# Kernel tuning notes

Hardware: AMD Instinct MI355X
Metric: run time of the kernel (lower is better)

Reference implementation:

```python
import jax, jax.numpy as jnp
import numpy as np

N_NODES = 50000
N_EDGES = 800000
F_IN = 128
HIDDEN = 128
N_CLASSES = 40


def setup_inputs() -> dict:
    key = jax.random.key(0)
    ks = jax.random.split(key, 8)
    x = jax.random.normal(ks[0], (N_NODES, F_IN), dtype=jnp.float32)
    edge_index = jax.random.randint(ks[1], (2, N_EDGES), 0, N_NODES, dtype=jnp.int32)
    s_in = 1.0 / np.sqrt(F_IN)
    s_h = 1.0 / np.sqrt(HIDDEN)
    W1_l = jax.random.normal(ks[2], (F_IN, HIDDEN), jnp.float32) * s_in
    W1_r = jax.random.normal(ks[3], (F_IN, HIDDEN), jnp.float32) * s_in
    b1 = jnp.zeros((HIDDEN,), jnp.float32)
    W2_l = jax.random.normal(ks[4], (HIDDEN, N_CLASSES), jnp.float32) * s_h
    W2_r = jax.random.normal(ks[5], (HIDDEN, N_CLASSES), jnp.float32) * s_h
    b2 = jnp.zeros((N_CLASSES,), jnp.float32)
    return {"x": x, "edge_index": edge_index, "W1_l": W1_l, "W1_r": W1_r,
            "b1": b1, "W2_l": W2_l, "W2_r": W2_r, "b2": b2}


def _sage_conv(x, src, dst, W_l, W_r, b):
    # mean-aggregate neighbor features at dst, then linear transform + root weight
    msg = x[src]                                                  # [E, d] gather
    agg = jax.ops.segment_sum(msg, dst, num_segments=N_NODES)     # [N, d] scatter-add
    deg = jax.ops.segment_sum(jnp.ones((src.shape[0],), x.dtype), dst,
                              num_segments=N_NODES)
    agg = agg / jnp.maximum(deg, 1.0)[:, None]                    # mean aggregation
    return agg @ W_l + x @ W_r + b


def reference(x, edge_index, W1_l, W1_r, b1, W2_l, W2_r, b2):
    src, dst = edge_index[0], edge_index[1]
    h = jax.nn.relu(_sage_conv(x, src, dst, W1_l, W1_r, b1))
    # F.dropout(p=0.5, training=self.training) -> identity in eval mode
    out = jax.nn.relu(_sage_conv(h, src, dst, W2_l, W2_r, b2))
    return jax.nn.log_softmax(out, axis=-1)
```

## Files before the change

kernel.cpp:

```cpp
#include <hip/hip_runtime.h>

#define N_NODES 50000
#define N_EDGES 800000
#define F_IN 128
#define HIDDEN 128
#define N_CLASSES 40

#define NBUCKET 391
#define BUCKET_CAP 4096
#define BINA_CHUNK 2048
#define BINA_NBLK 391
#define PREP_ITEMS (N_NODES * 32 + 128 * 256 + 80 * 128)
#define PREP_NBLK (PREP_ITEMS / 256)

#define OFF_RS     0
#define OFF_BCNT   50004
#define OFF_INVDEG 100004
#define OFF_SRCS   150004
#define OFF_AB     950004
#define OFF_PB     950004
#define OFF_Q      2950004
#define OFF_BINS   7350004
#define OFF_WT1    10550004
#define OFF_WT2    10566388

typedef short bf16x8 __attribute__((ext_vector_type(8)));
typedef float f32x4 __attribute__((ext_vector_type(4)));
typedef unsigned short u16x8 __attribute__((ext_vector_type(8)));

static __device__ __forceinline__ unsigned short f2bf(float f) {
  unsigned int u = __builtin_bit_cast(unsigned int, f);
  u = (u + 0x7fffu + ((u >> 16) & 1u)) >> 16;
  return (unsigned short)u;
}
static __device__ __forceinline__ float bf2f(unsigned short s) {
  unsigned int u = ((unsigned int)s) << 16;
  return __builtin_bit_cast(float, u);
}

__global__ __launch_bounds__(256) void k_binA_prep(
    const int* __restrict__ src, const int* __restrict__ dst,
    int* __restrict__ bcnt, int* __restrict__ bins,
    const float* __restrict__ x, const float* __restrict__ W1l,
    const float* __restrict__ W1r, const float* __restrict__ W2l,
    const float* __restrict__ W2r, unsigned short* __restrict__ Ab,
    unsigned short* __restrict__ Wt1, unsigned short* __restrict__ Wt2) {
  if (blockIdx.x >= BINA_NBLK) {
    int idx = (blockIdx.x - BINA_NBLK) * 256 + threadIdx.x;
    if (idx < N_NODES * 32) {
      int row = idx >> 5, c4 = (idx & 31) << 2;
      const float4 v = *(const float4*)(x + (size_t)row * F_IN + c4);
      ushort4 o;
      o.x = f2bf(v.x); o.y = f2bf(v.y); o.z = f2bf(v.z); o.w = f2bf(v.w);
      *(ushort4*)(Ab + (size_t)row * 256 + 128 + c4) = o;
      return;
    }
    idx -= N_NODES * 32;
    if (idx < 128 * 256) {
      int n = idx >> 8, k = idx & 255;
      float v = (k < 128) ? W1l[(size_t)k * 128 + n]
                          : W1r[(size_t)(k - 128) * 128 + n];
      Wt1[(size_t)n * 256 + k] = f2bf(v);
    } else if (idx < 128 * 256 + 80 * 128) {
      int j = idx - 128 * 256;
      int n = j >> 7, k = j & 127;
      float v = (n < 40) ? W2l[(size_t)k * 40 + n]
                         : W2r[(size_t)k * 40 + (n - 40)];
      Wt2[(size_t)n * 128 + k] = f2bf(v);
    }
    return;
  }
  __shared__ int cnt[NBUCKET];
  __shared__ int excl[NBUCKET];
  __shared__ int cursor[NBUCKET];
  __shared__ int bbase[NBUCKET];
  __shared__ int sc[256];
  __shared__ int stage[BINA_CHUNK];
  __shared__ unsigned short bkt[BINA_CHUNK];
  int t = threadIdx.x;
  int e0 = blockIdx.x * BINA_CHUNK;
  int ne = N_EDGES - e0;
  if (ne > BINA_CHUNK) ne = BINA_CHUNK;
  for (int i = t; i < NBUCKET; i += 256) cnt[i] = 0;
  __syncthreads();
  for (int i = t; i < ne; i += 256) atomicAdd(&cnt[dst[e0 + i] >> 7], 1);
  __syncthreads();
  int a = (2 * t < NBUCKET) ? cnt[2 * t] : 0;
  int b2_ = (2 * t + 1 < NBUCKET) ? cnt[2 * t + 1] : 0;
  int s = a + b2_;
  sc[t] = s;
  __syncthreads();
  for (int off = 1; off < 256; off <<= 1) {
    int add = (t >= off) ? sc[t - off] : 0;
    __syncthreads();
    sc[t] += add;
    __syncthreads();
  }
  int pbase = sc[t] - s;
  if (2 * t < NBUCKET) { excl[2 * t] = pbase; cursor[2 * t] = pbase; }
  if (2 * t + 1 < NBUCKET) {
    excl[2 * t + 1] = pbase + a;
    cursor[2 * t + 1] = pbase + a;
  }
  for (int i = t; i < NBUCKET; i += 256)
    bbase[i] = atomicAdd(&bcnt[i], cnt[i]);
  __syncthreads();
  for (int i = t; i < ne; i += 256) {
    int d = dst[e0 + i];
    int sv = src[e0 + i];
    int b = d >> 7;
    int pos = atomicAdd(&cursor[b], 1);
    stage[pos] = ((d & 127) << 16) | sv;
    bkt[pos] = (unsigned short)b;
  }
  __syncthreads();
  for (int i = t; i < ne; i += 256) {
    int b = bkt[i];
    bins[(size_t)b * BUCKET_CAP + bbase[b] + (i - excl[b])] = stage[i];
  }
}

__global__ __launch_bounds__(256) void k_binB(
    const int* __restrict__ bcnt, const int* __restrict__ bins,
    int* __restrict__ rs, int* __restrict__ srcs,
    float* __restrict__ invdeg) {
  __shared__ int sc[256];
  __shared__ int hist[128];
  __shared__ int cursor[128];
  int b = blockIdx.x;
  int t = threadIdx.x;
  int v = 0;
  if (t < b) v += bcnt[t];
  if (t + 256 < b) v += bcnt[t + 256];
  sc[t] = v;
  __syncthreads();
  for (int off = 128; off; off >>= 1) {
    if (t < off) sc[t] += sc[t + off];
    __syncthreads();
  }
  int base = sc[0];
  int cnt = bcnt[b];
  const int* bb = bins + (size_t)b * BUCKET_CAP;
  if (t < 128) hist[t] = 0;
  __syncthreads();
  for (int i = t; i < cnt; i += 256) atomicAdd(&hist[bb[i] >> 16], 1);
  __syncthreads();
  int c = (t < 128) ? hist[t] : 0;
  sc[t] = c;
  __syncthreads();
  for (int off = 1; off < 128; off <<= 1) {
    int add = (t >= off) ? sc[t - off] : 0;
    __syncthreads();
    sc[t] += add;
    __syncthreads();
  }
  int lexcl = sc[t] - c;
  int node = b * 128 + t;
  if (t < 128 && node < N_NODES) {
    rs[node] = base + lexcl;
    invdeg[node] = 1.0f / (float)(c > 1 ? c : 1);
  }
  if (b == 0 && t == 0) rs[N_NODES] = N_EDGES;
  if (t < 128) cursor[t] = lexcl;
  __syncthreads();
  for (int i = t; i < cnt; i += 256) {
    int v2 = bb[i];
    int pos = atomicAdd(&cursor[v2 >> 16], 1);
    srcs[base + pos] = v2 & 0xFFFF;
  }
}

__global__ __launch_bounds__(256) void k_gather1(
    const int* __restrict__ rs, const int* __restrict__ srcs,
    const float* __restrict__ invdeg, unsigned short* __restrict__ Ab) {
  int node = blockIdx.x * 4 + (threadIdx.x >> 6);
  int lane = threadIdx.x & 63;
  int slot = lane >> 3, li = lane & 7;
  if (node >= N_NODES) return;
  int beg = rs[node], end = rs[node + 1];
  float acc[16];
#pragma unroll
  for (int j = 0; j < 16; j++) acc[j] = 0.f;
  for (int i = beg + slot; i < end; i += 8) {
    int s = srcs[i];
    const unsigned short* rp = Ab + (size_t)s * 256 + 128 + li * 8;
    u16x8 v0 = *(const u16x8*)rp;
    u16x8 v1 = *(const u16x8*)(rp + 64);
#pragma unroll
    for (int j = 0; j < 8; j++) {
      acc[j] += bf2f(v0[j]);
      acc[8 + j] += bf2f(v1[j]);
    }
  }
#pragma unroll
  for (int off = 8; off <= 32; off <<= 1)
#pragma unroll
    for (int j = 0; j < 16; j++) acc[j] += __shfl_xor(acc[j], off, 64);
  if (slot == 0) {
    float inv = invdeg[node];
    u16x8 o0, o1;
#pragma unroll
    for (int j = 0; j < 8; j++) {
      o0[j] = f2bf(acc[j] * inv);
      o1[j] = f2bf(acc[8 + j] * inv);
    }
    *(u16x8*)(Ab + (size_t)node * 256 + li * 8) = o0;
    *(u16x8*)(Ab + (size_t)node * 256 + 64 + li * 8) = o1;
  }
}

__global__ __launch_bounds__(256) void k_mlp(
    const unsigned short* __restrict__ Ab, const unsigned short* __restrict__ Wt1,
    const unsigned short* __restrict__ Wt2, const float* __restrict__ b1,
    const float* __restrict__ b2, unsigned short* __restrict__ pb,
    float* __restrict__ q) {
  __shared__ unsigned short hs[64 * 132];
  int w = threadIdx.x >> 6, lane = threadIdx.x & 63;
  int r = lane & 15, quad = lane >> 4;
  int row0 = blockIdx.x * 64 + w * 16;
  int arow = row0 + r;
  if (arow >= N_NODES) arow = N_NODES - 1;
  const unsigned short* Ap = Ab + (size_t)arow * 256 + quad * 8;
  const unsigned short* Bp = Wt1 + (size_t)r * 256 + quad * 8;
  f32x4 acc[8];
#pragma unroll
  for (int n = 0; n < 8; n++) acc[n] = (f32x4){0.f, 0.f, 0.f, 0.f};
#pragma unroll
  for (int k0 = 0; k0 < 256; k0 += 32) {
    bf16x8 af = *(const bf16x8*)(Ap + k0);
#pragma unroll
    for (int n = 0; n < 8; n++) {
      bf16x8 bv = *(const bf16x8*)(Bp + (size_t)n * 16 * 256 + k0);
      acc[n] = __builtin_amdgcn_mfma_f32_16x16x32_bf16(af, bv, acc[n], 0, 0, 0);
    }
  }
  int lrow0 = w * 16 + quad * 4;
#pragma unroll
  for (int n = 0; n < 8; n++) {
    int col = n * 16 + r;
    float bias = b1[col];
#pragma unroll
    for (int reg = 0; reg < 4; reg++)
      hs[(lrow0 + reg) * 132 + col] = f2bf(fmaxf(acc[n][reg] + bias, 0.f));
  }
  __syncthreads();
  int lr = w * 16 + r;
  const unsigned short* Bp2 = Wt2 + (size_t)r * 128 + quad * 8;
  f32x4 acc2[5];
#pragma unroll
  for (int n = 0; n < 5; n++) acc2[n] = (f32x4){0.f, 0.f, 0.f, 0.f};
#pragma unroll
  for (int k0 = 0; k0 < 128; k0 += 32) {
    const unsigned short* hp = &hs[lr * 132 + k0 + quad * 8];
    ushort4 h0 = *(const ushort4*)hp;
    ushort4 h1 = *(const ushort4*)(hp + 4);
    bf16x8 af;
    af[0] = (short)h0.x; af[1] = (short)h0.y; af[2] = (short)h0.z; af[3] = (short)h0.w;
    af[4] = (short)h1.x; af[5] = (short)h1.y; af[6] = (short)h1.z; af[7] = (short)h1.w;
#pragma unroll
    for (int n = 0; n < 5; n++) {
      bf16x8 bv = *(const bf16x8*)(Bp2 + (size_t)n * 16 * 128 + k0);
      acc2[n] = __builtin_amdgcn_mfma_f32_16x16x32_bf16(af, bv, acc2[n], 0, 0, 0);
    }
  }
  int crow0 = row0 + quad * 4;
#pragma unroll
  for (int n = 0; n < 5; n++) {
    int col = n * 16 + r;
#pragma unroll
    for (int reg = 0; reg < 4; reg++) {
      int row = crow0 + reg;
      if (row < N_NODES) {
        float v = acc2[n][reg];
        if (col < N_CLASSES)
          pb[(size_t)row * 40 + col] = f2bf(v);
        else
          q[(size_t)row * N_CLASSES + (col - N_CLASSES)] = v + b2[col - N_CLASSES];
      }
    }
  }
}

__global__ __launch_bounds__(256) void k_final(
    const unsigned short* __restrict__ pb, const float* __restrict__ q,
    const int* __restrict__ rs, const int* __restrict__ srcs,
    const float* __restrict__ invdeg, float* __restrict__ out) {
  int node = blockIdx.x * 4 + (threadIdx.x >> 6);
  int lane = threadIdx.x & 63;
  int slot = lane >> 3, li = lane & 7;
  if (node >= N_NODES) return;
  bool valid = li < 5;
  int beg = rs[node], end = rs[node + 1];
  float acc[8];
#pragma unroll
  for (int j = 0; j < 8; j++) acc[j] = 0.f;
  for (int i = beg + slot; i < end; i += 8) {
    int s = srcs[i];
    if (valid) {
      u16x8 v = *(const u16x8*)(pb + (size_t)s * 40 + li * 8);
#pragma unroll
      for (int j = 0; j < 8; j++) acc[j] += bf2f(v[j]);
    }
  }
#pragma unroll
  for (int off = 8; off <= 32; off <<= 1)
#pragma unroll
    for (int j = 0; j < 8; j++) acc[j] += __shfl_xor(acc[j], off, 64);
  float inv = invdeg[node];
  float v[8];
  float m = -1e30f;
  if (valid) {
    const float* qr = q + (size_t)node * N_CLASSES + li * 8;
    float4 q0 = *(const float4*)qr;
    float4 q1 = *(const float4*)(qr + 4);
    v[0] = fmaxf(acc[0] * inv + q0.x, 0.f);
    v[1] = fmaxf(acc[1] * inv + q0.y, 0.f);
    v[2] = fmaxf(acc[2] * inv + q0.z, 0.f);
    v[3] = fmaxf(acc[3] * inv + q0.w, 0.f);
    v[4] = fmaxf(acc[4] * inv + q1.x, 0.f);
    v[5] = fmaxf(acc[5] * inv + q1.y, 0.f);
    v[6] = fmaxf(acc[6] * inv + q1.z, 0.f);
    v[7] = fmaxf(acc[7] * inv + q1.w, 0.f);
#pragma unroll
    for (int j = 0; j < 8; j++) m = fmaxf(m, v[j]);
  }
#pragma unroll
  for (int off = 1; off <= 4; off <<= 1) m = fmaxf(m, __shfl_xor(m, off, 8));
  float ssum = 0.f;
  if (valid) {
#pragma unroll
    for (int j = 0; j < 8; j++) ssum += __expf(v[j] - m);
  }
#pragma unroll
  for (int off = 1; off <= 4; off <<= 1) ssum += __shfl_xor(ssum, off, 8);
  float lse = __logf(ssum) + m;
  if (slot == 0 && valid) {
    float* orow = out + (size_t)node * N_CLASSES + li * 8;
    *(float4*)orow = make_float4(v[0] - lse, v[1] - lse, v[2] - lse, v[3] - lse);
    *(float4*)(orow + 4) =
        make_float4(v[4] - lse, v[5] - lse, v[6] - lse, v[7] - lse);
  }
}

extern "C" void kernel_launch(void* const* d_in, const int* in_sizes, int n_in,
                              void* d_out, int out_size, void* d_ws,
                              size_t ws_size, hipStream_t stream) {
  const float* x   = (const float*)d_in[0];
  const int*   ei  = (const int*)d_in[1];
  const int*   src = ei;
  const int*   dst = ei + N_EDGES;
  const float* W1l = (const float*)d_in[2];
  const float* W1r = (const float*)d_in[3];
  const float* b1  = (const float*)d_in[4];
  const float* W2l = (const float*)d_in[5];
  const float* W2r = (const float*)d_in[6];
  const float* b2  = (const float*)d_in[7];
  float* out = (float*)d_out;

  float* wsf = (float*)d_ws;
  int*   rs     = (int*)wsf + OFF_RS;
  int*   bcnt   = (int*)wsf + OFF_BCNT;
  float* invdeg = wsf + OFF_INVDEG;
  int*   srcs   = (int*)wsf + OFF_SRCS;
  unsigned short* Ab  = (unsigned short*)(wsf + OFF_AB);
  unsigned short* pb  = (unsigned short*)(wsf + OFF_PB);
  unsigned short* Wt1 = (unsigned short*)(wsf + OFF_WT1);
  unsigned short* Wt2 = (unsigned short*)(wsf + OFF_WT2);
  int*   bins   = (int*)wsf + OFF_BINS;
  float* q = wsf + OFF_Q;

  hipMemsetAsync(bcnt, 0, NBUCKET * sizeof(int), stream);

  k_binA_prep<<<BINA_NBLK + PREP_NBLK, 256, 0, stream>>>(
      src, dst, bcnt, bins, x, W1l, W1r, W2l, W2r, Ab, Wt1, Wt2);
  k_binB<<<NBUCKET, 256, 0, stream>>>(bcnt, bins, rs, srcs, invdeg);
  k_gather1<<<(N_NODES + 3) / 4, 256, 0, stream>>>(rs, srcs, invdeg, Ab);
  k_mlp<<<(N_NODES + 63) / 64, 256, 0, stream>>>(Ab, Wt1, Wt2, b1, b2, pb, q);
  k_final<<<(N_NODES + 3) / 4, 256, 0, stream>>>(pb, q, rs, srcs, invdeg, out);
}
```

Measured before the change: 233.4 us.

## Retile MLP kernel across waves by column and move pb/q off Ab

The fused MLP kernel now handles 32 rows per block, with each wave computing two 16-column tiles for both 16-row tiles. This cuts per-wave weight fragment loads and doubles the block count. The second-layer GEMM is split across waves by row tile and column group. The pb and q outputs move from a region aliasing the Ab input into the spent bins region, which removes a cross-block read/write overlap.

After: 223.2 us. 1.05x faster.

```diff
diff --git a/kernel.cpp b/kernel.cpp
--- a/kernel.cpp
+++ b/kernel.cpp
@@ -18,9 +18,9 @@
 #define OFF_INVDEG 100004
 #define OFF_SRCS   150004
 #define OFF_AB     950004
-#define OFF_PB     950004
-#define OFF_Q      2950004
 #define OFF_BINS   7350004
+#define OFF_PB     7350004
+#define OFF_Q      8350004
 #define OFF_WT1    10550004
 #define OFF_WT2    10566388
 
@@ -214,68 +214,83 @@
     const unsigned short* __restrict__ Wt2, const float* __restrict__ b1,
     const float* __restrict__ b2, unsigned short* __restrict__ pb,
     float* __restrict__ q) {
-  __shared__ unsigned short hs[64 * 132];
+  __shared__ unsigned short hs[32 * 132];
   int w = threadIdx.x >> 6, lane = threadIdx.x & 63;
   int r = lane & 15, quad = lane >> 4;
-  int row0 = blockIdx.x * 64 + w * 16;
-  int arow = row0 + r;
-  if (arow >= N_NODES) arow = N_NODES - 1;
-  const unsigned short* Ap = Ab + (size_t)arow * 256 + quad * 8;
-  const unsigned short* Bp = Wt1 + (size_t)r * 256 + quad * 8;
-  f32x4 acc[8];
-#pragma unroll
-  for (int n = 0; n < 8; n++) acc[n] = (f32x4){0.f, 0.f, 0.f, 0.f};
+  int row0 = blockIdx.x * 32;
+  int ar0 = row0 + r;
+  int ar1 = row0 + 16 + r;
+  if (ar0 >= N_NODES) ar0 = N_NODES - 1;
+  if (ar1 >= N_NODES) ar1 = N_NODES - 1;
+  const unsigned short* Ap0 = Ab + (size_t)ar0 * 256 + quad * 8;
+  const unsigned short* Ap1 = Ab + (size_t)ar1 * 256 + quad * 8;
+  const unsigned short* Bp = Wt1 + (size_t)(w * 32 + r) * 256 + quad * 8;
+  f32x4 acc[2][2];
+#pragma unroll
+  for (int nn = 0; nn < 2; nn++)
+#pragma unroll
+    for (int rt = 0; rt < 2; rt++) acc[nn][rt] = (f32x4){0.f, 0.f, 0.f, 0.f};
 #pragma unroll
   for (int k0 = 0; k0 < 256; k0 += 32) {
-    bf16x8 af = *(const bf16x8*)(Ap + k0);
-#pragma unroll
-    for (int n = 0; n < 8; n++) {
-      bf16x8 bv = *(const bf16x8*)(Bp + (size_t)n * 16 * 256 + k0);
-      acc[n] = __builtin_amdgcn_mfma_f32_16x16x32_bf16(af, bv, acc[n], 0, 0, 0);
-    }
-  }
-  int lrow0 = w * 16 + quad * 4;
-#pragma unroll
-  for (int n = 0; n < 8; n++) {
-    int col = n * 16 + r;
+    bf16x8 a0 = *(const bf16x8*)(Ap0 + k0);
+    bf16x8 a1 = *(const bf16x8*)(Ap1 + k0);
+#pragma unroll
+    for (int nn = 0; nn < 2; nn++) {
+      bf16x8 bv = *(const bf16x8*)(Bp + (size_t)nn * 16 * 256 + k0);
+      acc[nn][0] = __builtin_amdgcn_mfma_f32_16x16x32_bf16(a0, bv, acc[nn][0], 0, 0, 0);
+      acc[nn][1] = __builtin_amdgcn_mfma_f32_16x16x32_bf16(a1, bv, acc[nn][1], 0, 0, 0);
+    }
+  }
+#pragma unroll
+  for (int nn = 0; nn < 2; nn++) {
+    int col = (w * 2 + nn) * 16 + r;
     float bias = b1[col];
 #pragma unroll
-    for (int reg = 0; reg < 4; reg++)
-      hs[(lrow0 + reg) * 132 + col] = f2bf(fmaxf(acc[n][reg] + bias, 0.f));
-  }
-  __syncthreads();
-  int lr = w * 16 + r;
-  const unsigned short* Bp2 = Wt2 + (size_t)r * 128 + quad * 8;
-  f32x4 acc2[5];
-#pragma unroll
-  for (int n = 0; n < 5; n++) acc2[n] = (f32x4){0.f, 0.f, 0.f, 0.f};
+    for (int rt = 0; rt < 2; rt++)
+#pragma unroll
+      for (int reg = 0; reg < 4; reg++)
+        hs[(rt * 16 + quad * 4 + reg) * 132 + col] =
+            f2bf(fmaxf(acc[nn][rt][reg] + bias, 0.f));
+  }
+  __syncthreads();
+  int rt2 = w & 1, ng = w >> 1;
+  int nbeg = ng ? 3 : 0;
+  int ncnt = ng ? 2 : 3;
+  const unsigned short* hrow = hs + (rt2 * 16 + r) * 132 + quad * 8;
+  const unsigned short* Bp2 = Wt2 + (size_t)(nbeg * 16 + r) * 128 + quad * 8;
+  f32x4 acc2[3];
+#pragma unroll
+  for (int j = 0; j < 3; j++) acc2[j] = (f32x4){0.f, 0.f, 0.f, 0.f};
 #pragma unroll
   for (int k0 = 0; k0 < 128; k0 += 32) {
-    const unsigned short* hp = &hs[lr * 132 + k0 + quad * 8];
-    ushort4 h0 = *(const ushort4*)hp;
-    ushort4 h1 = *(const ushort4*)(hp + 4);
+    ushort4 h0 = *(const ushort4*)(hrow + k0);
+    ushort4 h1 = *(const ushort4*)(hrow + k0 + 4);
     bf16x8 af;
     af[0] = (short)h0.x; af[1] = (short)h0.y; af[2] = (short)h0.z; af[3] = (short)h0.w;
     af[4] = (short)h1.x; af[5] = (short)h1.y; af[6] = (short)h1.z; af[7] = (short)h1.w;
 #pragma unroll
-    for (int n = 0; n < 5; n++) {
-      bf16x8 bv = *(const bf16x8*)(Bp2 + (size_t)n * 16 * 128 + k0);
-      acc2[n] = __builtin_amdgcn_mfma_f32_16x16x32_bf16(af, bv, acc2[n], 0, 0, 0);
-    }
-  }
-  int crow0 = row0 + quad * 4;
-#pragma unroll
-  for (int n = 0; n < 5; n++) {
-    int col = n * 16 + r;
-#pragma unroll
-    for (int reg = 0; reg < 4; reg++) {
-      int row = crow0 + reg;
-      if (row < N_NODES) {
-        float v = acc2[n][reg];
-        if (col < N_CLASSES)
-          pb[(size_t)row * 40 + col] = f2bf(v);
-        else
-          q[(size_t)row * N_CLASSES + (col - N_CLASSES)] = v + b2[col - N_CLASSES];
+    for (int j = 0; j < 3; j++) {
+      if (j < ncnt) {
+        bf16x8 bv = *(const bf16x8*)(Bp2 + (size_t)j * 16 * 128 + k0);
+        acc2[j] = __builtin_amdgcn_mfma_f32_16x16x32_bf16(af, bv, acc2[j], 0, 0, 0);
+      }
+    }
+  }
+  int crow0 = row0 + rt2 * 16 + quad * 4;
+#pragma unroll
+  for (int j = 0; j < 3; j++) {
+    if (j < ncnt) {
+      int col = (nbeg + j) * 16 + r;
+#pragma unroll
+      for (int reg = 0; reg < 4; reg++) {
+        int row = crow0 + reg;
+        if (row < N_NODES) {
+          float v = acc2[j][reg];
+          if (col < N_CLASSES)
+            pb[(size_t)row * 40 + col] = f2bf(v);
+          else
+            q[(size_t)row * N_CLASSES + (col - N_CLASSES)] = v + b2[col - N_CLASSES];
+        }
       }
     }
   }
@@ -375,6 +390,6 @@
       src, dst, bcnt, bins, x, W1l, W1r, W2l, W2r, Ab, Wt1, Wt2);
   k_binB<<<NBUCKET, 256, 0, stream>>>(bcnt, bins, rs, srcs, invdeg);
   k_gather1<<<(N_NODES + 3) / 4, 256, 0, stream>>>(rs, srcs, invdeg, Ab);
-  k_mlp<<<(N_NODES + 63) / 64, 256, 0, stream>>>(Ab, Wt1, Wt2, b1, b2, pb, q);
+  k_mlp<<<(N_NODES + 31) / 32, 256, 0, stream>>>(Ab, Wt1, Wt2, b1, b2, pb, q);
   k_final<<<(N_NODES + 3) / 4, 256, 0, stream>>>(pb, q, rs, srcs, invdeg, out);
 }
```
